# Performance work log

Measured on AMD Instinct MI355X. Metric: run time of the kernel, lower is better.

The kernel has to match this reference:

```python
import jax, jax.numpy as jnp
import numpy as np


def setup_inputs() -> dict:
    key = jax.random.key(0)
    k1, k2, k3 = jax.random.split(key, 3)
    B, H, S, D = 1, 16, 2048, 64
    NPOS, HID = 64, 1024
    query = jax.random.normal(k1, (B, H, S, D), dtype=jnp.float32)
    attn_logits = jax.random.normal(k2, (B, H, S, S), dtype=jnp.float32)
    pos_emb = jax.random.normal(k3, (1, NPOS, HID), dtype=jnp.float32)
    return {"query": query, "attn_logits": attn_logits, "pos_emb": pos_emb}


def reference(query, attn_logits, pos_emb):
    # query: [B,H,S,D]; attn_logits: [B,H,S,S]; pos_emb: [1,NPOS,H*D]
    B, H, S, D = query.shape
    npos_max = pos_emb.shape[1]
    gates = jax.nn.sigmoid(attn_logits)
    # reverse cumsum along keys: position of each key relative to query
    pos = jnp.flip(jnp.cumsum(jnp.flip(gates, axis=-1), axis=-1), axis=-1)
    pos = jnp.minimum(pos, npos_max - 1)
    pos_ceil = jnp.ceil(pos).astype(jnp.int32)
    pos_floor = jnp.floor(pos).astype(jnp.int32)
    # split heads: [1,NPOS,H*D] -> [H,NPOS,D]
    pe = pos_emb.reshape(npos_max, H, D).transpose(1, 0, 2)
    # per-head position logits: [B,H,S,NPOS]
    logits_int = jnp.einsum('bhsd,hnd->bhsn', query, pe)
    logits_ceil = jnp.take_along_axis(logits_int, pos_ceil, axis=-1)
    logits_floor = jnp.take_along_axis(logits_int, pos_floor, axis=-1)
    w = pos - pos_floor  # fractional interpolation weight
    return logits_ceil * w + logits_floor * (1.0 - w)
```

## Files before the change

kernel.cpp:

```cpp
#include <hip/hip_runtime.h>

namespace {
constexpr int kH       = 16;
constexpr int kS       = 2048;
constexpr int kD       = 64;
constexpr int kNpos    = 64;
constexpr int kHid     = 1024;
constexpr int kChunk   = 256;
constexpr int kNChunks = kS / kChunk;
constexpr int kRowsPerBlock = 16;
}

typedef float vfloat4 __attribute__((ext_vector_type(4)));

__device__ __forceinline__ float dot4f(float4 a, float qx, float qy, float qz, float qw) {
    return fmaf(a.x, qx, fmaf(a.y, qy, fmaf(a.z, qz, a.w * qw)));
}

template <int CTRL, int ROWM>
__device__ __forceinline__ float dpp_add(float v) {
    int t = __builtin_amdgcn_update_dpp(0, __float_as_int(v), CTRL, ROWM, 0xf, true);
    return v + __int_as_float(t);
}

__device__ __forceinline__ float wave_incl_scan(float v) {
    v = dpp_add<0x111, 0xf>(v);
    v = dpp_add<0x112, 0xf>(v);
    v = dpp_add<0x114, 0xf>(v);
    v = dpp_add<0x118, 0xf>(v);
    v = dpp_add<0x142, 0xa>(v);
    v = dpp_add<0x143, 0xc>(v);
    return v;
}

__device__ __forceinline__ float bcast_lane(float v, int l) {
    return __int_as_float(__builtin_amdgcn_readlane(__float_as_int(v), l));
}

__device__ __forceinline__ void nt_store4(float* p, float a, float b, float c, float d) {
    vfloat4 v = {a, b, c, d};
    __builtin_nontemporal_store(v, reinterpret_cast<vfloat4*>(p));
}
__device__ __forceinline__ vfloat4 nt_load4(const float* p) {
    return __builtin_nontemporal_load(reinterpret_cast<const vfloat4*>(p));
}

__device__ __forceinline__ float sigm(float v) {
    return 1.0f / (1.0f + __expf(-v));
}

__device__ __forceinline__ float interp1(float acc, float pin) {
    float pc = fminf(pin, 63.0f);
    float fl = floorf(pc);
    float w  = pc - fl;
    int  fi  = (int)fl;
    int  ni  = (fi < kNpos - 1) ? fi + 1 : kNpos - 1;
    float lf = __shfl(acc, fi);
    float ln = __shfl(acc, ni);
    return fmaf(w, ln - lf, lf);
}

__device__ __forceinline__ void fill_row(float* __restrict__ orow,
                                         float fill, int lane) {
    #pragma unroll
    for (int j = 0; j < kNChunks - 1; ++j) {
        nt_store4(orow + j * kChunk + lane * 4, fill, fill, fill, fill);
    }
}

__device__ __forceinline__ void scan_row(const float* __restrict__ arow,
                                         float* __restrict__ orow,
                                         float acc, vfloat4 x0, int lane) {
    float running = 0.0f;
    vfloat4 x = x0;
    for (int c = kNChunks - 1; c >= 0; --c) {
        if (c != kNChunks - 1)
            x = nt_load4(arow + c * kChunk + lane * 4);
        float g0 = sigm(x.x), g1 = sigm(x.y);
        float g2 = sigm(x.z), g3 = sigm(x.w);

        float e3 = g3;
        float e2 = e3 + g2;
        float e1 = e2 + g1;
        float e0 = e1 + g0;

        float incl  = wave_incl_scan(e0);
        float total = bcast_lane(incl, 63);
        float sfx   = running + (total - incl);

        float r0 = interp1(acc, sfx + e0);
        float r1 = interp1(acc, sfx + e1);
        float r2 = interp1(acc, sfx + e2);
        float r3 = interp1(acc, sfx + e3);
        nt_store4(orow + c * kChunk + lane * 4, r0, r1, r2, r3);

        running += total;
        if (running >= 63.0f) break;
    }
}

__global__ __launch_bounds__(256) void cope_kernel(
    const float* __restrict__ query,
    const float* __restrict__ attn,
    const float* __restrict__ pos_emb,
    float* __restrict__ out)
{
    const int t    = threadIdx.x;
    const int lane = t & 63;
    const int wid  = t >> 6;
    const int row_base = blockIdx.x * kRowsPerBlock;
    const int h        = row_base >> 11;
    const int wrow = __builtin_amdgcn_readfirstlane(row_base + wid * 4);

    __shared__ float4 pe_lds[kNpos * 16];

    const float* arow = attn + (size_t)wrow * kS;
    float*       orow = out  + (size_t)wrow * kS;

    const int tail = (kNChunks - 1) * kChunk + lane * 4;
    vfloat4 x0 = nt_load4(arow + 0 * kS + tail);
    vfloat4 x1 = nt_load4(arow + 1 * kS + tail);
    vfloat4 x2 = nt_load4(arow + 2 * kS + tail);
    vfloat4 x3 = nt_load4(arow + 3 * kS + tail);

    #pragma unroll
    for (int k = 0; k < 4; ++k) {
        const int e = t + 256 * k;
        const int n = e >> 4;
        const int j = e & 15;
        float4 p = *reinterpret_cast<const float4*>(
            pos_emb + (size_t)n * kHid + h * kD + 4 * j);
        pe_lds[(n << 4) | (j ^ (n & 15))] = p;
    }
    __syncthreads();

    const float* qbase = query + (size_t)wrow * kD;
    float acc0 = 0.f, acc1 = 0.f, acc2 = 0.f, acc3 = 0.f;
    #pragma unroll 4
    for (int j = 0; j < 16; ++j) {
        float4 pe4 = pe_lds[(lane << 4) | (j ^ (lane & 15))];
        const float* q0 = qbase + 0 * kD + 4 * j;
        const float* q1 = qbase + 1 * kD + 4 * j;
        const float* q2 = qbase + 2 * kD + 4 * j;
        const float* q3 = qbase + 3 * kD + 4 * j;
        acc0 += dot4f(pe4, q0[0], q0[1], q0[2], q0[3]);
        acc1 += dot4f(pe4, q1[0], q1[1], q1[2], q1[3]);
        acc2 += dot4f(pe4, q2[0], q2[1], q2[2], q2[3]);
        acc3 += dot4f(pe4, q3[0], q3[1], q3[2], q3[3]);
    }

    fill_row(orow + 0 * kS, bcast_lane(acc0, kNpos - 1), lane);
    fill_row(orow + 1 * kS, bcast_lane(acc1, kNpos - 1), lane);
    fill_row(orow + 2 * kS, bcast_lane(acc2, kNpos - 1), lane);
    fill_row(orow + 3 * kS, bcast_lane(acc3, kNpos - 1), lane);

    scan_row(arow + 0 * kS, orow + 0 * kS, acc0, x0, lane);
    scan_row(arow + 1 * kS, orow + 1 * kS, acc1, x1, lane);
    scan_row(arow + 2 * kS, orow + 2 * kS, acc2, x2, lane);
    scan_row(arow + 3 * kS, orow + 3 * kS, acc3, x3, lane);
}

extern "C" void kernel_launch(void* const* d_in, const int* in_sizes, int n_in,
                              void* d_out, int out_size, void* d_ws, size_t ws_size,
                              hipStream_t stream) {
    const float* query   = (const float*)d_in[0];
    const float* attn    = (const float*)d_in[1];
    const float* pos_emb = (const float*)d_in[2];
    float* out = (float*)d_out;

    const int rows = kH * kS;
    dim3 grid(rows / kRowsPerBlock), block(256);
    cope_kernel<<<grid, block, 0, stream>>>(query, attn, pos_emb, out);
}
```

Measured before the change: 57.82 us.

## Split constant-fill stores into a separate kernel ahead of the scan kernel

The bulk constant fill of the clamped prefix of each output row moves out of the scan kernel into its own kernel. That kernel computes only the dot product of the query with position embedding 63, using a wave reduction, then streams the fill stores. The scan kernel then handles just the reverse cumsum and interpolation of the tail chunks, overwriting the filled region where needed. The aim is to decouple the pure store traffic from the scan dependency chain. The cost is a second launch and rewriting the last chunk twice.

```diff
diff --git a/kernel.cpp b/kernel.cpp
--- a/kernel.cpp
+++ b/kernel.cpp
@@ -37,6 +37,10 @@
     return __int_as_float(__builtin_amdgcn_readlane(__float_as_int(v), l));
 }
 
+__device__ __forceinline__ float wave_sum(float v) {
+    return bcast_lane(wave_incl_scan(v), 63);
+}
+
 __device__ __forceinline__ void nt_store4(float* p, float a, float b, float c, float d) {
     vfloat4 v = {a, b, c, d};
     __builtin_nontemporal_store(v, reinterpret_cast<vfloat4*>(p));
@@ -60,11 +64,34 @@
     return fmaf(w, ln - lf, lf);
 }
 
-__device__ __forceinline__ void fill_row(float* __restrict__ orow,
-                                         float fill, int lane) {
+__global__ __launch_bounds__(256) void cope_fill_kernel(
+    const float* __restrict__ query,
+    const float* __restrict__ pos_emb,
+    float* __restrict__ out)
+{
+    const int t    = threadIdx.x;
+    const int lane = t & 63;
+    const int wid  = t >> 6;
+    const int row_base = blockIdx.x * kRowsPerBlock;
+    const int h        = row_base >> 11;
+    const int wrow = __builtin_amdgcn_readfirstlane(row_base + wid * 4);
+
+    const float pe63 = pos_emb[(size_t)(kNpos - 1) * kHid + h * kD + lane];
+
+    const float* qrow = query + (size_t)wrow * kD;
+    const float f0 = wave_sum(qrow[0 * kD + lane] * pe63);
+    const float f1 = wave_sum(qrow[1 * kD + lane] * pe63);
+    const float f2 = wave_sum(qrow[2 * kD + lane] * pe63);
+    const float f3 = wave_sum(qrow[3 * kD + lane] * pe63);
+
+    float* orow = out + (size_t)wrow * kS;
     #pragma unroll
     for (int j = 0; j < kNChunks - 1; ++j) {
-        nt_store4(orow + j * kChunk + lane * 4, fill, fill, fill, fill);
+        const int off = j * kChunk + lane * 4;
+        nt_store4(orow + 0 * kS + off, f0, f0, f0, f0);
+        nt_store4(orow + 1 * kS + off, f1, f1, f1, f1);
+        nt_store4(orow + 2 * kS + off, f2, f2, f2, f2);
+        nt_store4(orow + 3 * kS + off, f3, f3, f3, f3);
     }
 }
 
@@ -99,7 +126,7 @@
     }
 }
 
-__global__ __launch_bounds__(256) void cope_kernel(
+__global__ __launch_bounds__(256) void cope_tail_kernel(
     const float* __restrict__ query,
     const float* __restrict__ attn,
     const float* __restrict__ pos_emb,
@@ -149,11 +176,6 @@
         acc3 += dot4f(pe4, q3[0], q3[1], q3[2], q3[3]);
     }
 
-    fill_row(orow + 0 * kS, bcast_lane(acc0, kNpos - 1), lane);
-    fill_row(orow + 1 * kS, bcast_lane(acc1, kNpos - 1), lane);
-    fill_row(orow + 2 * kS, bcast_lane(acc2, kNpos - 1), lane);
-    fill_row(orow + 3 * kS, bcast_lane(acc3, kNpos - 1), lane);
-
     scan_row(arow + 0 * kS, orow + 0 * kS, acc0, x0, lane);
     scan_row(arow + 1 * kS, orow + 1 * kS, acc1, x1, lane);
     scan_row(arow + 2 * kS, orow + 2 * kS, acc2, x2, lane);
@@ -170,5 +192,7 @@
 
     const int rows = kH * kS;
     dim3 grid(rows / kRowsPerBlock), block(256);
-    cope_kernel<<<grid, block, 0, stream>>>(query, attn, pos_emb, out);
+
+    cope_fill_kernel<<<grid, block, 0, stream>>>(query, pos_emb, out);
+    cope_tail_kernel<<<grid, block, 0, stream>>>(query, attn, pos_emb, out);
 }
```

After: 62.48 us. 8.1% more time.
